# Kernel optimization log

Measured on AMD Instinct MI355X. Metric: run time of the kernel, lower is better.

## Reference

```python
import jax, jax.numpy as jnp
import numpy as np

B, C, N, K = 2, 128, 4096, 16
DIM, PH, AH = 256, 64, 1024  # dim, pos_hidden_dim, dim*attn_hidden_multiplier
EPS = 1e-5

def _p(k, shape, scale=0.02):
    return jax.random.normal(k, shape, dtype=jnp.float32) * scale

def setup_inputs() -> dict:
    key0 = jax.random.key(0)
    ks = jax.random.split(key0, 32)
    d = {
        'pos': jax.random.normal(ks[0], (B, 3, N), dtype=jnp.float32),
        'key': jax.random.normal(ks[1], (B, C, N), dtype=jnp.float32),
        'query': jax.random.normal(ks[2], (B, C, N), dtype=jnp.float32),
        # MLP_Res on concat(key,query): in=2C, hidden=C, out=C
        'mlpv_w1': _p(ks[3], (C, 2 * C)), 'mlpv_b1': jnp.zeros((C,)),
        'mlpv_w2': _p(ks[4], (C, C)),     'mlpv_b2': jnp.zeros((C,)),
        'mlpv_ws': _p(ks[5], (C, 2 * C)), 'mlpv_bs': jnp.zeros((C,)),
        'wk': _p(ks[6], (DIM, C)), 'bk': jnp.zeros((DIM,)),
        'wq': _p(ks[7], (DIM, C)), 'bq': jnp.zeros((DIM,)),
        'wv': _p(ks[8], (DIM, C)), 'bv': jnp.zeros((DIM,)),
        # pos_mlp: Conv2d(3,PH,1) -> BN -> ReLU -> Conv2d(PH,DIM,1)
        'pos_w1': _p(ks[9], (PH, 3)),   'pos_b1': jnp.zeros((PH,)),
        'pos_g1': jnp.ones((PH,)),      'pos_be1': jnp.zeros((PH,)),
        'pos_w2': _p(ks[10], (DIM, PH)),'pos_b2': jnp.zeros((DIM,)),
        # attn_mlp: Conv2d(DIM,AH,1) -> BN -> ReLU -> Conv2d(AH,DIM,1)
        'att_w1': _p(ks[11], (AH, DIM)), 'att_b1': jnp.zeros((AH,)),
        'att_g1': jnp.ones((AH,)),       'att_be1': jnp.zeros((AH,)),
        'att_w2': _p(ks[12], (DIM, AH)), 'att_b2': jnp.zeros((DIM,)),
        'we': _p(ks[13], (C, DIM)), 'be': jnp.zeros((C,)),
    }
    return d

def conv1d(w, b, x):  # 1x1 conv: (o,i),(B,i,N)->(B,o,N)
    return jnp.einsum('oi,bin->bon', w, x) + b[None, :, None]

def conv2d(w, b, x):  # 1x1 conv: (o,i),(B,i,N,K)->(B,o,N,K)
    return jnp.einsum('oi,bink->bonk', w, x) + b[None, :, None, None]

def bn2d(g, be, x):  # training-mode batchnorm over (B,N,K) per channel
    m = x.mean(axis=(0, 2, 3), keepdims=True)
    v = x.var(axis=(0, 2, 3), keepdims=True)
    return g[None, :, None, None] * (x - m) * jax.lax.rsqrt(v + EPS) + be[None, :, None, None]

def knn_idx(pos, k):  # pos: (B,3,N) -> idx (B,N,k) of k nearest (incl. self)
    sq = jnp.sum(pos * pos, axis=1)                      # (B,N)
    d2 = sq[:, :, None] + sq[:, None, :] - 2.0 * jnp.einsum('bdn,bdm->bnm', pos, pos)
    _, idx = jax.lax.top_k(-d2, k)                       # smallest distances
    return idx

def group(x, idx):  # x:(B,C,N), idx:(B,N,K) -> (B,C,N,K)
    return jax.vmap(lambda xb, ib: xb[:, ib])(x, idx)

def reference(pos, key, query,
              mlpv_w1, mlpv_b1, mlpv_w2, mlpv_b2, mlpv_ws, mlpv_bs,
              wk, bk, wq, bq, wv, bv,
              pos_w1, pos_b1, pos_g1, pos_be1, pos_w2, pos_b2,
              att_w1, att_b1, att_g1, att_be1, att_w2, att_b2,
              we, be):
    x = jnp.concatenate([key, query], axis=1)            # (B,2C,N)
    value = conv1d(mlpv_w2, mlpv_b2, jax.nn.relu(conv1d(mlpv_w1, mlpv_b1, x))) \
            + conv1d(mlpv_ws, mlpv_bs, x)                # MLP_Res -> (B,C,N)
    identity = value
    k_f = conv1d(wk, bk, key)                            # (B,DIM,N)
    q_f = conv1d(wq, bq, query)
    v_f = conv1d(wv, bv, value)
    idx = knn_idx(pos, K)                                # (B,N,K)
    key_g = group(k_f, idx)                              # (B,DIM,N,K)
    qk_rel = q_f[:, :, :, None] - key_g
    pos_rel = pos[:, :, :, None] - group(pos, idx)       # (B,3,N,K)
    pos_emb = conv2d(pos_w2, pos_b2,
                     jax.nn.relu(bn2d(pos_g1, pos_be1, conv2d(pos_w1, pos_b1, pos_rel))))
    attn = conv2d(att_w2, att_b2,
                  jax.nn.relu(bn2d(att_g1, att_be1, conv2d(att_w1, att_b1, qk_rel + pos_emb))))
    attn = jax.nn.softmax(attn, axis=-1)                 # softmax over K neighbors
    v = v_f[:, :, :, None] + pos_emb                     # (B,DIM,N,K)
    agg = jnp.einsum('bcik,bcik->bci', attn, v)          # (B,DIM,N)
    y = conv1d(we, be, agg)
    return y + identity
```

## Files before the change

kernel.cpp:

```cpp
#include <hip/hip_runtime.h>
#include <math.h>

#define BB 2
#define CC 128
#define NN 4096
#define KK 16
#define DIMD 256
#define PHH 64
#define AHH 1024
#define EPSF 1e-5f
#define RSPLIT 256
#define RKCH ((BB * NN * KK) / RSPLIT)
#define LSTR 258
#define KNN_CAP 512
#define FPT 8

typedef unsigned short ushort_t;
typedef unsigned char uchar_t;
typedef unsigned long long u64;
typedef long long i64;
typedef __attribute__((ext_vector_type(8))) short short8;
typedef __attribute__((ext_vector_type(8))) unsigned short u16x8;
typedef __attribute__((ext_vector_type(4))) unsigned short u16x4;
typedef __attribute__((ext_vector_type(2))) unsigned short u16x2;
typedef __attribute__((ext_vector_type(4))) float f32x4;

__device__ __forceinline__ ushort_t f2b(float x) {
    union { float f; unsigned u; } v; v.f = x;
    unsigned r = v.u + 0x7fff + ((v.u >> 16) & 1);
    return (ushort_t)(r >> 16);
}
__device__ __forceinline__ float b2f(ushort_t x) {
    union { unsigned u; float f; } v; v.u = ((unsigned)x) << 16;
    return v.f;
}
__device__ __forceinline__ unsigned fsort(float x) {
    union { float f; unsigned u; } v; v.f = x;
    return v.u ^ ((v.u >> 31) ? 0xFFFFFFFFu : 0x80000000u);
}
__device__ __forceinline__ uchar_t f2f8(float x) {
    int p = __builtin_amdgcn_cvt_pk_fp8_f32(x, x, 0, false);
    return (uchar_t)(p & 0xFF);
}

#define GLDS16(gp, lp) __builtin_amdgcn_global_load_lds( \
    (const __attribute__((address_space(1))) void*)(gp), \
    (__attribute__((address_space(3))) void*)(lp), 16, 0, 0)

__global__ void zero_kernel(float* p, int n) {
    int i = blockIdx.x * blockDim.x + threadIdx.x;
    if (i < n) p[i] = 0.f;
}

__global__ __launch_bounds__(256) void knn_kernel(const float* __restrict__ pos,
                                                  int* __restrict__ idx) {
    int bid = blockIdx.x;
    int b = bid / NN, n = bid % NN;
    int t = threadIdx.x;
    int lane = t & 63, w = t >> 6;
    const float* px = pos + (size_t)b * 3 * NN;
    const float* py = px + NN;
    const float* pz = px + 2 * NN;
    float qx = px[n], qy = py[n], qz = pz[n];
    float qs = qx * qx + qy * qy + qz * qz;

    u64 keys[KK];
    u64 lmin = ~0ull;
#pragma unroll
    for (int j = 0; j < KK; ++j) {
        int m = t + 256 * j;
        float mx = px[m], my = py[m], mz = pz[m];
        float ms = mx * mx + my * my + mz * mz;
        float dt = qx * mx + qy * my + qz * mz;
        float d = qs + ms - 2.f * dt;
        u64 k = ((u64)fsort(d) << 32) | (unsigned)m;
        keys[j] = k;
        lmin = k < lmin ? k : lmin;
    }

    __shared__ u64 T0s[4];
    __shared__ u64 pool[KNN_CAP];
    __shared__ int cnt;

    u64 k = lmin, m4 = 0;
#pragma unroll
    for (int r = 0; r < 4; ++r) {
        u64 mv = k;
#pragma unroll
        for (int off = 32; off >= 1; off >>= 1) {
            u64 o = __shfl_xor(mv, off);
            mv = o < mv ? o : mv;
        }
        if (r == 3) m4 = mv;
        if (k == mv) k = ~0ull;
    }
    if (lane == 0) T0s[w] = m4;
    if (t == 0) cnt = 0;
    __syncthreads();
    u64 T0 = T0s[0];
    T0 = T0s[1] > T0 ? T0s[1] : T0;
    T0 = T0s[2] > T0 ? T0s[2] : T0;
    T0 = T0s[3] > T0 ? T0s[3] : T0;

#pragma unroll
    for (int j = 0; j < KK; ++j) {
        if (keys[j] <= T0) {
            int p = atomicAdd(&cnt, 1);
            if (p < KNN_CAP) pool[p] = keys[j];
        }
    }
    __syncthreads();
    int C = cnt < KNN_CAP ? cnt : KNN_CAP;
    if (t < C) {
        u64 me = pool[t];
        int r = 0;
        for (int i = 0; i < C; ++i) r += (pool[i] < me);
        if (r < KK) idx[(size_t)bid * KK + r] = (int)(me & 0xFFFFFFFFu);
    }
}

__global__ __launch_bounds__(256) void cvtx_kernel(const float* __restrict__ key,
                                                   const float* __restrict__ query,
                                                   ushort_t* __restrict__ kqT) {
    __shared__ float xs[128][65];
    int b = blockIdx.y, n0 = blockIdx.x * 64, t = threadIdx.x;
    for (int h = 0; h < 2; ++h) {
        const float* src = (h ? query : key) + (size_t)b * CC * NN;
        if (h) __syncthreads();
#pragma unroll
        for (int it = 0; it < 32; ++it) {
            int l = it * 256 + t;
            xs[l >> 6][l & 63] = src[(size_t)(l >> 6) * NN + n0 + (l & 63)];
        }
        __syncthreads();
#pragma unroll
        for (int it = 0; it < 8; ++it) {
            int l = it * 256 + t;
            int row = l >> 5, c0 = (l & 31) * 4;
            u16x4 pk;
            pk[0] = f2b(xs[c0][row]);
            pk[1] = f2b(xs[c0 + 1][row]);
            pk[2] = f2b(xs[c0 + 2][row]);
            pk[3] = f2b(xs[c0 + 3][row]);
            *(u16x4*)(kqT + ((size_t)b * NN + n0 + row) * 256 + h * 128 + c0) = pk;
        }
    }
}

template <int KLOOP, int ASTR, int EPI, int OSTR>
__global__ __launch_bounds__(256) void gemmT_kernel(const ushort_t* __restrict__ A,
                                                    const ushort_t* __restrict__ Bm,
                                                    const float* __restrict__ bias,
                                                    float* __restrict__ outF,
                                                    ushort_t* __restrict__ outB) {
    __shared__ ushort_t lA[128 * 32];
    __shared__ ushort_t lB[128 * 32];
    int t = threadIdx.x, lane = t & 63, w = t >> 6;
    int wr = w >> 1, wc = w & 1;
    size_t row0 = (size_t)blockIdx.x * 128;
    int col0 = blockIdx.y * 128;
    int m16 = lane & 15, kg = lane >> 4;
    f32x4 acc[4][4];
#pragma unroll
    for (int i = 0; i < 4; ++i)
#pragma unroll
        for (int j = 0; j < 4; ++j) acc[i][j] = (f32x4){0.f, 0.f, 0.f, 0.f};

    const ushort_t* gA = A + (row0 + (size_t)w * 16 + m16) * ASTR + kg * 8;
    const ushort_t* gB = Bm + ((size_t)(col0 + w * 16 + m16)) * KLOOP + kg * 8;
    ushort_t* lA0 = lA + w * 512;
    ushort_t* lB0 = lB + w * 512;
    for (int kt = 0; kt < KLOOP / 32; ++kt) {
        int ko = kt * 32;
        GLDS16(gA + ko, lA0);
        GLDS16(gA + (size_t)64 * ASTR + ko, lA0 + 2048);
        GLDS16(gB + ko, lB0);
        GLDS16(gB + (size_t)64 * KLOOP + ko, lB0 + 2048);
        __syncthreads();
        short8 af[4], bf[4];
#pragma unroll
        for (int i = 0; i < 4; ++i) {
            af[i] = *(const short8*)(lA + ((wr * 4 + i) * 512 + kg * 128 + m16 * 8));
            bf[i] = *(const short8*)(lB + ((wc * 4 + i) * 512 + kg * 128 + m16 * 8));
        }
#pragma unroll
        for (int i = 0; i < 4; ++i)
#pragma unroll
            for (int j = 0; j < 4; ++j)
                acc[i][j] = __builtin_amdgcn_mfma_f32_16x16x32_bf16(af[i], bf[j], acc[i][j], 0, 0, 0);
        __syncthreads();
    }
#pragma unroll
    for (int j = 0; j < 4; ++j) {
        int n = col0 + wc * 64 + j * 16 + m16;
        float bi = bias[n];
#pragma unroll
        for (int i = 0; i < 4; ++i) {
            size_t r = row0 + wr * 64 + i * 16 + kg * 4;
#pragma unroll
            for (int rg = 0; rg < 4; ++rg) {
                float v = acc[i][j][rg] + bi;
                if (EPI == 0) outB[(r + rg) * (size_t)OSTR + n] = f2b(fmaxf(v, 0.f));
                else          outF[(r + rg) * (size_t)OSTR + n] = v;
            }
        }
    }
}

__global__ __launch_bounds__(256) void gemmval_kernel(const ushort_t* __restrict__ kqT,
                                                      const ushort_t* __restrict__ h1T,
                                                      const ushort_t* __restrict__ wsb,
                                                      const ushort_t* __restrict__ w2vb,
                                                      const float* __restrict__ b2,
                                                      const float* __restrict__ bs,
                                                      float* __restrict__ valueTf,
                                                      ushort_t* __restrict__ valueTb) {
    __shared__ ushort_t lA[128 * 32];
    __shared__ ushort_t lB[128 * 32];
    int t = threadIdx.x, lane = t & 63, w = t >> 6;
    int wr = w >> 1, wc = w & 1;
    size_t row0 = (size_t)blockIdx.x * 128;
    int m16 = lane & 15, kg = lane >> 4;
    f32x4 acc[4][4];
#pragma unroll
    for (int i = 0; i < 4; ++i)
#pragma unroll
        for (int j = 0; j < 4; ++j) acc[i][j] = (f32x4){0.f, 0.f, 0.f, 0.f};
    ushort_t* lA0 = lA + w * 512;
    ushort_t* lB0 = lB + w * 512;

    {
        const ushort_t* gA = kqT + (row0 + (size_t)w * 16 + m16) * 256 + kg * 8;
        const ushort_t* gB = wsb + ((size_t)(w * 16 + m16)) * 256 + kg * 8;
        for (int kt = 0; kt < 8; ++kt) {
            int ko = kt * 32;
            GLDS16(gA + ko, lA0);
            GLDS16(gA + (size_t)64 * 256 + ko, lA0 + 2048);
            GLDS16(gB + ko, lB0);
            GLDS16(gB + (size_t)64 * 256 + ko, lB0 + 2048);
            __syncthreads();
            short8 af[4], bf[4];
#pragma unroll
            for (int i = 0; i < 4; ++i) {
                af[i] = *(const short8*)(lA + ((wr * 4 + i) * 512 + kg * 128 + m16 * 8));
                bf[i] = *(const short8*)(lB + ((wc * 4 + i) * 512 + kg * 128 + m16 * 8));
            }
#pragma unroll
            for (int i = 0; i < 4; ++i)
#pragma unroll
                for (int j = 0; j < 4; ++j)
                    acc[i][j] = __builtin_amdgcn_mfma_f32_16x16x32_bf16(af[i], bf[j], acc[i][j], 0, 0, 0);
            __syncthreads();
        }
    }
    {
        const ushort_t* gA = h1T + (row0 + (size_t)w * 16 + m16) * 128 + kg * 8;
        const ushort_t* gB = w2vb + ((size_t)(w * 16 + m16)) * 128 + kg * 8;
        for (int kt = 0; kt < 4; ++kt) {
            int ko = kt * 32;
            GLDS16(gA + ko, lA0);
            GLDS16(gA + (size_t)64 * 128 + ko, lA0 + 2048);
            GLDS16(gB + ko, lB0);
            GLDS16(gB + (size_t)64 * 128 + ko, lB0 + 2048);
            __syncthreads();
            short8 af[4], bf[4];
#pragma unroll
            for (int i = 0; i < 4; ++i) {
                af[i] = *(const short8*)(lA + ((wr * 4 + i) * 512 + kg * 128 + m16 * 8));
                bf[i] = *(const short8*)(lB + ((wc * 4 + i) * 512 + kg * 128 + m16 * 8));
            }
#pragma unroll
            for (int i = 0; i < 4; ++i)
#pragma unroll
                for (int j = 0; j < 4; ++j)
                    acc[i][j] = __builtin_amdgcn_mfma_f32_16x16x32_bf16(af[i], bf[j], acc[i][j], 0, 0, 0);
            __syncthreads();
        }
    }
#pragma unroll
    for (int j = 0; j < 4; ++j) {
        int n = wc * 64 + j * 16 + m16;
        float bi = b2[n] + bs[n];
#pragma unroll
        for (int i = 0; i < 4; ++i) {
            size_t r = row0 + wr * 64 + i * 16 + kg * 4;
#pragma unroll
            for (int rg = 0; rg < 4; ++rg) {
                float v = acc[i][j][rg] + bi;
                valueTf[(r + rg) * (size_t)CC + n] = v;
                valueTb[(r + rg) * (size_t)CC + n] = f2b(v);
            }
        }
    }
}

__global__ __launch_bounds__(256) void gemmkq_kernel(const ushort_t* __restrict__ kqT,
                                                     const ushort_t* __restrict__ wkb,
                                                     const ushort_t* __restrict__ wqb,
                                                     const float* __restrict__ bk,
                                                     const float* __restrict__ bq,
                                                     float* __restrict__ kT,
                                                     float* __restrict__ qT) {
    __shared__ ushort_t lA[128 * 32];
    __shared__ ushort_t lB[128 * 32];
    int half = blockIdx.y >> 1;
    int col0 = (blockIdx.y & 1) * 128;
    const ushort_t* A = kqT + half * 128;
    const ushort_t* Bm = half ? wqb : wkb;
    const float* bias = half ? bq : bk;
    float* outF = half ? qT : kT;

    int t = threadIdx.x, lane = t & 63, w = t >> 6;
    int wr = w >> 1, wc = w & 1;
    size_t row0 = (size_t)blockIdx.x * 128;
    int m16 = lane & 15, kg = lane >> 4;
    f32x4 acc[4][4];
#pragma unroll
    for (int i = 0; i < 4; ++i)
#pragma unroll
        for (int j = 0; j < 4; ++j) acc[i][j] = (f32x4){0.f, 0.f, 0.f, 0.f};
    const ushort_t* gA = A + (row0 + (size_t)w * 16 + m16) * 256 + kg * 8;
    const ushort_t* gB = Bm + ((size_t)(col0 + w * 16 + m16)) * 128 + kg * 8;
    ushort_t* lA0 = lA + w * 512;
    ushort_t* lB0 = lB + w * 512;
    for (int kt = 0; kt < 4; ++kt) {
        int ko = kt * 32;
        GLDS16(gA + ko, lA0);
        GLDS16(gA + (size_t)64 * 256 + ko, lA0 + 2048);
        GLDS16(gB + ko, lB0);
        GLDS16(gB + (size_t)64 * 128 + ko, lB0 + 2048);
        __syncthreads();
        short8 af[4], bf[4];
#pragma unroll
        for (int i = 0; i < 4; ++i) {
            af[i] = *(const short8*)(lA + ((wr * 4 + i) * 512 + kg * 128 + m16 * 8));
            bf[i] = *(const short8*)(lB + ((wc * 4 + i) * 512 + kg * 128 + m16 * 8));
        }
#pragma unroll
        for (int i = 0; i < 4; ++i)
#pragma unroll
            for (int j = 0; j < 4; ++j)
                acc[i][j] = __builtin_amdgcn_mfma_f32_16x16x32_bf16(af[i], bf[j], acc[i][j], 0, 0, 0);
        __syncthreads();
    }
#pragma unroll
    for (int j = 0; j < 4; ++j) {
        int n = col0 + wc * 64 + j * 16 + m16;
        float bi = bias[n];
#pragma unroll
        for (int i = 0; i < 4; ++i) {
            size_t r = row0 + wr * 64 + i * 16 + kg * 4;
#pragma unroll
            for (int rg = 0; rg < 4; ++rg)
                outF[(r + rg) * (size_t)DIMD + n] = acc[i][j][rg] + bi;
        }
    }
}

__global__ __launch_bounds__(256) void pos_stats_kernel(const float* __restrict__ pos,
                                                        const int* __restrict__ idx,
                                                        float* __restrict__ stats) {
    int sid = blockIdx.x * 256 + threadIdx.x;
    int b = sid / (NN * KK);
    int r = sid % (NN * KK);
    int n = r / KK;
    int m = idx[sid];
    const float* px = pos + (size_t)b * 3 * NN;
    float dx = px[n] - px[m];
    float dy = px[NN + n] - px[NN + m];
    float dz = px[2 * NN + n] - px[2 * NN + m];
    float v[9] = {dx, dy, dz, dx * dx, dy * dy, dz * dz, dx * dy, dx * dz, dy * dz};
    __shared__ float red[256];
    for (int j = 0; j < 9; ++j) {
        red[threadIdx.x] = v[j];
        __syncthreads();
        for (int off = 128; off >= 1; off >>= 1) {
            if (threadIdx.x < off) red[threadIdx.x] += red[threadIdx.x + off];
            __syncthreads();
        }
        if (threadIdx.x == 0) atomicAdd(&stats[j], red[0]);
        __syncthreads();
    }
}

__global__ void pos_bn_kernel(const float* __restrict__ stats, const float* __restrict__ pw1,
                              const float* __restrict__ pb1, const float* __restrict__ pg1,
                              const float* __restrict__ pbe1, float* __restrict__ posA) {
    int c = threadIdx.x;
    if (c >= PHH) return;
    float M = (float)(BB * NN * KK);
    float mu0 = stats[0] / M, mu1 = stats[1] / M, mu2 = stats[2] / M;
    float E00 = stats[3] / M, E11 = stats[4] / M, E22 = stats[5] / M;
    float E01 = stats[6] / M, E02 = stats[7] / M, E12 = stats[8] / M;
    float w0 = pw1[c * 3], w1 = pw1[c * 3 + 1], w2 = pw1[c * 3 + 2];
    float wmu = w0 * mu0 + w1 * mu1 + w2 * mu2;
    float mean_h = wmu + pb1[c];
    float Eh2 = w0 * w0 * E00 + w1 * w1 * E11 + w2 * w2 * E22
              + 2.f * (w0 * w1 * E01 + w0 * w2 * E02 + w1 * w2 * E12)
              + 2.f * pb1[c] * wmu + pb1[c] * pb1[c];
    float var = Eh2 - mean_h * mean_h;
    float a1 = pg1[c] * rsqrtf(var + EPSF);
    posA[c] = a1;
    posA[PHH + c] = pbe1[c] - mean_h * a1;
}

__global__ __launch_bounds__(256) void p1_kernel(const float* __restrict__ pos,
                                                 const int* __restrict__ idx,
                                                 const float* __restrict__ pw1,
                                                 const float* __restrict__ pb1,
                                                 const float* __restrict__ posA,
                                                 ushort_t* __restrict__ p1) {
    int gid = blockIdx.x * 256 + threadIdx.x;
    int samp = gid >> 6, c = gid & 63;
    int p = samp >> 4;
    int b = p >> 12, n = p & (NN - 1);
    int m = idx[samp];
    const float* px = pos + (size_t)b * 3 * NN;
    float dx = px[n] - px[m];
    float dy = px[NN + n] - px[NN + m];
    float dz = px[2 * NN + n] - px[2 * NN + m];
    float h = pw1[c * 3] * dx + pw1[c * 3 + 1] * dy + pw1[c * 3 + 2] * dz + pb1[c];
    p1[gid] = f2b(fmaxf(h * posA[c] + posA[PHH + c], 0.f));
}

__global__ __launch_bounds__(1024) void rg_kernel(const ushort_t* __restrict__ S,
                                                  float* __restrict__ Rpart,
                                                  float* __restrict__ mu) {
    __shared__ ushort_t ls[32 * LSTR];
    __shared__ float fmu[DIMD];
    int t = threadIdx.x;
    int lane = t & 63, w = t >> 6;
    int ti = w >> 3, tj = (w >> 2) & 1;
    int wr = (w >> 1) & 1, wc = w & 1;
    int m16 = lane & 15, kg = lane >> 4;
    size_t kbase = (size_t)blockIdx.x * RKCH;

    if (t < DIMD) fmu[t] = 0.f;

    f32x4 acc[4][4];
#pragma unroll
    for (int i = 0; i < 4; ++i)
#pragma unroll
        for (int j = 0; j < 4; ++j) acc[i][j] = (f32x4){0.f, 0.f, 0.f, 0.f};

    int lm = t >> 5;
    int lc = (t & 31) * 8;
    const ushort_t* gS = S + (kbase + lm) * DIMD + lc;
    ushort_t* lp = ls + lm * LSTR + lc;
    float csum[8];
#pragma unroll
    for (int c = 0; c < 8; ++c) csum[c] = 0.f;

    for (int kt = 0; kt < RKCH / 32; ++kt) {
        u16x8 v = *(const u16x8*)(gS + (size_t)kt * 32 * DIMD);
        __syncthreads();
#pragma unroll
        for (int q = 0; q < 4; ++q)
            *(u16x2*)(lp + 2 * q) = (u16x2){v[2 * q], v[2 * q + 1]};
#pragma unroll
        for (int c = 0; c < 8; ++c) csum[c] += b2f(v[c]);
        __syncthreads();
        short8 af[4], bf[4];
#pragma unroll
        for (int i = 0; i < 4; ++i) {
            int chA = ti * 128 + wr * 64 + i * 16 + m16;
            int chB = tj * 128 + wc * 64 + i * 16 + m16;
#pragma unroll
            for (int j = 0; j < 8; ++j) {
                int k = kg * 8 + j;
                af[i][j] = (short)ls[k * LSTR + chA];
                bf[i][j] = (short)ls[k * LSTR + chB];
            }
        }
#pragma unroll
        for (int i = 0; i < 4; ++i)
#pragma unroll
            for (int j = 0; j < 4; ++j)
                acc[i][j] = __builtin_amdgcn_mfma_f32_16x16x32_bf16(af[i], bf[j], acc[i][j], 0, 0, 0);
    }

    float* rp = Rpart + (size_t)blockIdx.x * (DIMD * DIMD);
#pragma unroll
    for (int i = 0; i < 4; ++i) {
        int r0 = ti * 128 + wr * 64 + i * 16 + kg * 4;
#pragma unroll
        for (int j = 0; j < 4; ++j) {
            int cn = tj * 128 + wc * 64 + j * 16 + m16;
#pragma unroll
            for (int rg = 0; rg < 4; ++rg)
                rp[(size_t)(r0 + rg) * DIMD + cn] = acc[i][j][rg];
        }
    }

    __syncthreads();
#pragma unroll
    for (int c = 0; c < 8; ++c) atomicAdd(&fmu[lc + c], csum[c]);
    __syncthreads();
    if (t < DIMD) atomicAdd(&mu[t], fmu[t]);
}

__global__ __launch_bounds__(256) void r_reduce_kernel(const float* __restrict__ Rpart,
                                                       float* __restrict__ R) {
    int e = blockIdx.x * 256 + threadIdx.x;
    float s = 0.f;
    for (int p = 0; p < RSPLIT; ++p) s += Rpart[(size_t)p * (DIMD * DIMD) + e];
    R[e] = s;
}

__global__ __launch_bounds__(256) void attn_bn_kernel(const float* __restrict__ R,
                                                      const float* __restrict__ mu,
                                                      const float* __restrict__ aw1,
                                                      const float* __restrict__ ab1,
                                                      const float* __restrict__ ag1,
                                                      const float* __restrict__ abe1,
                                                      float* __restrict__ attA) {
    int c = blockIdx.x;
    int t = threadIdx.x;
    __shared__ float wsh[DIMD];
    __shared__ float red[DIMD];
    wsh[t] = aw1[(size_t)c * DIMD + t];
    __syncthreads();
    const float* Rr = R + (size_t)t * DIMD;
    float q = 0.f;
#pragma unroll 4
    for (int j = 0; j < DIMD; ++j) q += Rr[j] * wsh[j];
    red[t] = q * wsh[t];
    __syncthreads();
    for (int off = 128; off >= 1; off >>= 1) {
        if (t < off) red[t] += red[t + off];
        __syncthreads();
    }
    float wRw = red[0];
    __syncthreads();
    red[t] = wsh[t] * mu[t];
    __syncthreads();
    for (int off = 128; off >= 1; off >>= 1) {
        if (t < off) red[t] += red[t + off];
        __syncthreads();
    }
    if (t == 0) {
        float M = (float)(BB * NN * KK);
        float wmu = red[0] / M;
        float b1c = ab1[c];
        float Eh = wmu + b1c;
        float Eh2 = wRw / M + 2.f * b1c * wmu + b1c * b1c;
        float var = Eh2 - Eh * Eh;
        float a1 = ag1[c] * rsqrtf(var + EPSF);
        attA[c] = a1;
        attA[AHH + c] = a1 * b1c + abe1[c] - Eh * a1;
    }
}

__global__ void cvt_w_kernel(const float* __restrict__ aw1, const float* __restrict__ aw2,
                             const float* __restrict__ pw2,
                             const float* __restrict__ mw1, const float* __restrict__ mws,
                             const float* __restrict__ mw2,
                             const float* __restrict__ wk, const float* __restrict__ wq,
                             const float* __restrict__ wv,
                             ushort_t* __restrict__ w1b, ushort_t* __restrict__ w2b,
                             ushort_t* __restrict__ pw2b,
                             ushort_t* __restrict__ w1vb, ushort_t* __restrict__ wsvb,
                             ushort_t* __restrict__ w2vb,
                             ushort_t* __restrict__ wkb, ushort_t* __restrict__ wqb,
                             ushort_t* __restrict__ wvb,
                             uchar_t* __restrict__ w2f8) {
    int i = blockIdx.x * 256 + threadIdx.x;
    int o = i;
    if (o < 262144) { w1b[o] = f2b(aw1[o]); return; }   o -= 262144;
    if (o < 262144) { w2b[o] = f2b(aw2[o]); w2f8[o] = f2f8(aw2[o] * 64.f); return; } o -= 262144;
    if (o < 16384)  { pw2b[o] = f2b(pw2[o]); return; }  o -= 16384;
    if (o < 32768)  { w1vb[o] = f2b(mw1[o]); return; }  o -= 32768;
    if (o < 32768)  { wsvb[o] = f2b(mws[o]); return; }  o -= 32768;
    if (o < 16384)  { w2vb[o] = f2b(mw2[o]); return; }  o -= 16384;
    if (o < 32768)  { wkb[o] = f2b(wk[o]); return; }    o -= 32768;
    if (o < 32768)  { wqb[o] = f2b(wq[o]); return; }    o -= 32768;
    if (o < 32768)  { wvb[o] = f2b(wv[o]); }
}

template <int KDIM>
__global__ __launch_bounds__(256) void gemmS_kernel(const ushort_t* __restrict__ A,
                                                    const ushort_t* __restrict__ Bm,
                                                    const float* __restrict__ p0,
                                                    ushort_t* __restrict__ Sb,
                                                    const float* __restrict__ qT,
                                                    const float* __restrict__ kT,
                                                    const int* __restrict__ gidx) {
    __shared__ ushort_t lA[128 * 32];
    __shared__ ushort_t lB[128 * 32];
    int t = threadIdx.x;
    int lane = t & 63, w = t >> 6;
    int wr = w >> 1, wc = w & 1;
    size_t row0 = (size_t)blockIdx.x * 128;
    int col0 = blockIdx.y * 128;
    int m16 = lane & 15, kg = lane >> 4;

    f32x4 acc[4][4];
#pragma unroll
    for (int i = 0; i < 4; ++i)
#pragma unroll
        for (int j = 0; j < 4; ++j) acc[i][j] = (f32x4){0.f, 0.f, 0.f, 0.f};

    const ushort_t* gA = A + (row0 + (size_t)w * 16 + m16) * KDIM + kg * 8;
    const ushort_t* gB = Bm + ((size_t)(col0 + w * 16 + m16)) * KDIM + kg * 8;
    ushort_t* lA0 = lA + w * 512;
    ushort_t* lB0 = lB + w * 512;

    for (int kt = 0; kt < KDIM / 32; ++kt) {
        int ko = kt * 32;
        GLDS16(gA + ko, lA0);
        GLDS16(gA + (size_t)64 * KDIM + ko, lA0 + 2048);
        GLDS16(gB + ko, lB0);
        GLDS16(gB + (size_t)64 * KDIM + ko, lB0 + 2048);
        __syncthreads();
        short8 af[4], bf[4];
#pragma unroll
        for (int i = 0; i < 4; ++i) {
            af[i] = *(const short8*)(lA + ((wr * 4 + i) * 512 + kg * 128 + m16 * 8));
            bf[i] = *(const short8*)(lB + ((wc * 4 + i) * 512 + kg * 128 + m16 * 8));
        }
#pragma unroll
        for (int i = 0; i < 4; ++i)
#pragma unroll
            for (int j = 0; j < 4; ++j)
                acc[i][j] = __builtin_amdgcn_mfma_f32_16x16x32_bf16(af[i], bf[j], acc[i][j], 0, 0, 0);
        __syncthreads();
    }

    int nn[4]; float bi[4];
#pragma unroll
    for (int j = 0; j < 4; ++j) { nn[j] = col0 + wc * 64 + j * 16 + m16; bi[j] = p0[nn[j]]; }
#pragma unroll
    for (int i = 0; i < 4; ++i) {
        size_t r = row0 + wr * 64 + i * 16 + kg * 4;
#pragma unroll
        for (int rg = 0; rg < 4; ++rg) {
            size_t rr = r + rg;
            int p = (int)(rr >> 4);
            int krow = (p & ~(NN - 1)) + gidx[rr];
            const float* qrow = qT + (size_t)p * DIMD;
            const float* kro = kT + (size_t)krow * DIMD;
#pragma unroll
            for (int j = 0; j < 4; ++j) {
                float sv = qrow[nn[j]] - kro[nn[j]] + acc[i][j][rg] + bi[j];
                Sb[rr * (size_t)DIMD + nn[j]] = f2b(sv);
            }
        }
    }
}

__global__ __launch_bounds__(256, 3) void fused_mlp_kernel(const ushort_t* __restrict__ S,
                                                        const ushort_t* __restrict__ w1b,
                                                        const uchar_t* __restrict__ w2f8,
                                                        const float* __restrict__ attA,
                                                        const float* __restrict__ ab2,
                                                        const int* __restrict__ idx,
                                                        const float* __restrict__ qT,
                                                        const float* __restrict__ kT,
                                                        const float* __restrict__ vT,
                                                        float* __restrict__ aggT) {
    __shared__ char smem[49152];
    ushort_t* lS  = (ushort_t*)smem;
    uchar_t*  lHt = (uchar_t*)(smem + 32768);
    ushort_t* lgB = (ushort_t*)smem;

    int t = threadIdx.x;
    int lane = t & 63, w = t >> 6;
    int m16 = lane & 15, kg = lane >> 4;
    size_t row0 = (size_t)blockIdx.x * 64;

#pragma unroll
    for (int i = 0; i < 8; ++i) {
        int lb = w * 8 + i;
        int kt = lb >> 2, st = lb & 3;
        const ushort_t* gp = S + (row0 + st * 16 + m16) * DIMD + kt * 32 + kg * 8;
        GLDS16(gp, lS + lb * 512);
    }

    f32x4 acc2[4][4];
#pragma unroll
    for (int i = 0; i < 4; ++i)
#pragma unroll
        for (int j = 0; j < 4; ++j) acc2[i][j] = (f32x4){0.f, 0.f, 0.f, 0.f};

    __syncthreads();

    for (int jc = 0; jc < 8; ++jc) {
        uchar_t* lHb = lHt + (jc & 1) * 8192;
        f32x4 acc1[2][4];
#pragma unroll
        for (int hi = 0; hi < 2; ++hi)
#pragma unroll
            for (int sj = 0; sj < 4; ++sj) acc1[hi][sj] = (f32x4){0.f, 0.f, 0.f, 0.f};
        const ushort_t* wrow = w1b + ((size_t)(jc * 128 + w * 32 + m16)) * DIMD + kg * 8;
#pragma unroll
        for (int kt = 0; kt < 8; ++kt) {
            short8 af[2], bf[4];
            af[0] = *(const short8*)(wrow + kt * 32);
            af[1] = *(const short8*)(wrow + (size_t)16 * DIMD + kt * 32);
#pragma unroll
            for (int sj = 0; sj < 4; ++sj)
                bf[sj] = *(const short8*)(lS + (kt * 4 + sj) * 512 + kg * 128 + m16 * 8);
            __builtin_amdgcn_s_setprio(1);
#pragma unroll
            for (int hi = 0; hi < 2; ++hi)
#pragma unroll
                for (int sj = 0; sj < 4; ++sj)
                    acc1[hi][sj] = __builtin_amdgcn_mfma_f32_16x16x32_bf16(af[hi], bf[sj], acc1[hi][sj], 0, 0, 0);
            __builtin_amdgcn_s_setprio(0);
        }
#pragma unroll
        for (int hi = 0; hi < 2; ++hi) {
            float4 sc4 = *(const float4*)(attA + jc * 128 + w * 32 + hi * 16 + kg * 4);
            float4 of4 = *(const float4*)(attA + AHH + jc * 128 + w * 32 + hi * 16 + kg * 4);
#pragma unroll
            for (int sj = 0; sj < 4; ++sj) {
                float h0 = fmaxf(sc4.x * acc1[hi][sj][0] + of4.x, 0.f);
                float h1 = fmaxf(sc4.y * acc1[hi][sj][1] + of4.y, 0.f);
                float h2 = fmaxf(sc4.z * acc1[hi][sj][2] + of4.z, 0.f);
                float h3 = fmaxf(sc4.w * acc1[hi][sj][3] + of4.w, 0.f);
                int p01 = __builtin_amdgcn_cvt_pk_fp8_f32(h0, h1, 0, false);
                int pk = __builtin_amdgcn_cvt_pk_fp8_f32(h2, h3, p01, true);
                int ah = (w * 4 + sj) * 512 + (hi * 2 + (kg >> 1)) * 128 + m16 * 8 + (kg & 1) * 4;
                *(int*)(lHb + ah) = pk;
            }
        }
        __syncthreads();
#pragma unroll
        for (int gh = 0; gh < 2; ++gh) {
            i64 af2[8];
#pragma unroll
            for (int gq = 0; gq < 2; ++gq)
#pragma unroll
                for (int oi = 0; oi < 4; ++oi)
                    af2[gq * 4 + oi] = *(const i64*)(w2f8 + ((size_t)(w * 64 + oi * 16 + m16)) * AHH + jc * 128 + (gh * 2 + gq) * 32 + kg * 8);
#pragma unroll
            for (int gq = 0; gq < 2; ++gq) {
                i64 bf2[4];
#pragma unroll
                for (int sj = 0; sj < 4; ++sj)
                    bf2[sj] = *(const i64*)(lHb + ((gh * 2 + gq) * 4 + sj) * 512 + kg * 128 + m16 * 8);
                __builtin_amdgcn_s_setprio(1);
#pragma unroll
                for (int oi = 0; oi < 4; ++oi)
#pragma unroll
                    for (int sj = 0; sj < 4; ++sj)
                        acc2[oi][sj] = __builtin_amdgcn_mfma_f32_16x16x32_fp8_fp8(af2[gq * 4 + oi], bf2[sj], acc2[oi][sj], 0, 0, 0);
                __builtin_amdgcn_s_setprio(0);
            }
        }
    }
    __syncthreads();

    const float invsc = 0.015625f;
#pragma unroll
    for (int oi = 0; oi < 4; ++oi) {
        int ob = w * 64 + oi * 16 + kg * 4;
        float4 b2v = *(const float4*)(ab2 + ob);
#pragma unroll
        for (int sj = 0; sj < 4; ++sj) {
            int smp = sj * 16 + m16;
            lgB[(ob + 0) * 72 + smp] = f2b(acc2[oi][sj][0] * invsc + b2v.x);
            lgB[(ob + 1) * 72 + smp] = f2b(acc2[oi][sj][1] * invsc + b2v.y);
            lgB[(ob + 2) * 72 + smp] = f2b(acc2[oi][sj][2] * invsc + b2v.z);
            lgB[(ob + 3) * 72 + smp] = f2b(acc2[oi][sj][3] * invsc + b2v.w);
        }
    }
    __syncthreads();

    int out = t;
    for (int pt = 0; pt < 4; ++pt) {
        int pid = (int)(row0 >> 4) + pt;
        u16x8 v0 = *(const u16x8*)(lgB + out * 72 + pt * 16);
        u16x8 v1 = *(const u16x8*)(lgB + out * 72 + pt * 16 + 8);
        float lg[KK];
#pragma unroll
        for (int s = 0; s < 8; ++s) { lg[s] = b2f(v0[s]); lg[s + 8] = b2f(v1[s]); }
        float mx = lg[0];
#pragma unroll
        for (int s = 1; s < KK; ++s) mx = fmaxf(mx, lg[s]);
        float se = 0.f;
#pragma unroll
        for (int s = 0; s < KK; ++s) { lg[s] = expf(lg[s] - mx); se += lg[s]; }
        float inv = 1.f / se;
        int base = pid & ~(NN - 1);
        float acc = 0.f;
#pragma unroll
        for (int s = 0; s < KK; ++s) {
            int row = pid * KK + s;
            int krow = base + idx[row];
            float sv = b2f(S[(size_t)row * DIMD + out]);
            float kv = kT[(size_t)krow * DIMD + out];
            acc += lg[s] * (sv + kv);
        }
        float vf = vT[(size_t)pid * DIMD + out];
        float q  = qT[(size_t)pid * DIMD + out];
        aggT[(size_t)pid * DIMD + out] = vf - q + acc * inv;
    }
}

__global__ __launch_bounds__(256) void final_kernel(const float* __restrict__ aggT,
                                                    const float* __restrict__ we,
                                                    const float* __restrict__ be,
                                                    const float* __restrict__ valueTf,
                                                    float* __restrict__ out) {
    __shared__ float xs[2 * FPT][DIMD];
    __shared__ float vs[2 * FPT][CC];
    int b = blockIdx.y;
    int n0 = blockIdx.x * (2 * FPT);
    int t = threadIdx.x;
    const float4* src = (const float4*)(aggT + ((size_t)b * NN + n0) * DIMD);
    float4* dst = (float4*)xs;
#pragma unroll
    for (int l = 0; l < (2 * FPT * DIMD / 4) / 256; ++l) dst[t + 256 * l] = src[t + 256 * l];
    const float4* src2 = (const float4*)(valueTf + ((size_t)b * NN + n0) * CC);
    float4* dst2 = (float4*)vs;
#pragma unroll
    for (int l = 0; l < (2 * FPT * CC / 4) / 256; ++l) dst2[t + 256 * l] = src2[t + 256 * l];
    __syncthreads();
    int o = t & 127, ph = t >> 7;
    float acc[FPT];
#pragma unroll
    for (int p = 0; p < FPT; ++p) acc[p] = 0.f;
    const float4* wr = (const float4*)(we + (size_t)o * DIMD);
#pragma unroll 8
    for (int i4 = 0; i4 < DIMD / 4; ++i4) {
        float4 w4 = wr[i4];
#pragma unroll
        for (int p = 0; p < FPT; ++p) {
            float4 x4 = *(const float4*)&xs[ph * FPT + p][i4 * 4];
            acc[p] += w4.x * x4.x + w4.y * x4.y + w4.z * x4.z + w4.w * x4.w;
        }
    }
    float bo = be[o];
#pragma unroll
    for (int p = 0; p < FPT; ++p) {
        size_t oi = ((size_t)b * CC + o) * NN + n0 + ph * FPT + p;
        out[oi] = acc[p] + bo + vs[ph * FPT + p][o];
    }
}

extern "C" void kernel_launch(void* const* d_in, const int* in_sizes, int n_in,
                              void* d_out, int out_size, void* d_ws, size_t ws_size,
                              hipStream_t stream) {
    (void)in_sizes; (void)n_in; (void)out_size; (void)ws_size;
    const float* pos     = (const float*)d_in[0];
    const float* key     = (const float*)d_in[1];
    const float* query   = (const float*)d_in[2];
    const float* mlpv_w1 = (const float*)d_in[3];
    const float* mlpv_b1 = (const float*)d_in[4];
    const float* mlpv_w2 = (const float*)d_in[5];
    const float* mlpv_b2 = (const float*)d_in[6];
    const float* mlpv_ws = (const float*)d_in[7];
    const float* mlpv_bs = (const float*)d_in[8];
    const float* wk  = (const float*)d_in[9];
    const float* bk  = (const float*)d_in[10];
    const float* wq  = (const float*)d_in[11];
    const float* bq  = (const float*)d_in[12];
    const float* wv  = (const float*)d_in[13];
    const float* bv  = (const float*)d_in[14];
    const float* pw1 = (const float*)d_in[15];
    const float* pb1 = (const float*)d_in[16];
    const float* pg1 = (const float*)d_in[17];
    const float* pbe1= (const float*)d_in[18];
    const float* pw2 = (const float*)d_in[19];
    const float* pb2 = (const float*)d_in[20];
    const float* aw1 = (const float*)d_in[21];
    const float* ab1 = (const float*)d_in[22];
    const float* ag1 = (const float*)d_in[23];
    const float* abe1= (const float*)d_in[24];
    const float* aw2 = (const float*)d_in[25];
    const float* ab2 = (const float*)d_in[26];
    const float* we  = (const float*)d_in[27];
    const float* be  = (const float*)d_in[28];
    float* out = (float*)d_out;

    char* wsb = (char*)d_ws;
    size_t off = 0;
    auto alloc = [&](size_t bytes) {
        void* p = wsb + off;
        off += (bytes + 255) & ~(size_t)255;
        return p;
    };
    const size_t M = (size_t)BB * NN * KK;
    const size_t P = (size_t)BB * NN;
    int*   idx   = (int*)  alloc(M * 4);
    ushort_t* kqT     = (ushort_t*)alloc(P * 256 * 2);
    ushort_t* h1T     = (ushort_t*)alloc(P * CC * 2);
    float*    valueTf = (float*)   alloc(P * CC * 4);
    ushort_t* valueTb = (ushort_t*)alloc(P * CC * 2);
    float* kT    = (float*)alloc(P * DIMD * 4);
    float* qT    = (float*)alloc(P * DIMD * 4);
    float* vT    = (float*)alloc(P * DIMD * 4);
    float* aggT  = (float*)alloc(P * DIMD * 4);
    float* zero0 = (float*)alloc((size_t)(16 + 256 + 65536) * 4);
    float* stats = zero0;
    float* mu    = zero0 + 16;
    float* R     = zero0 + 16 + 256;
    float* posA  = (float*)alloc((size_t)2 * PHH * 4);
    float* attA  = (float*)alloc((size_t)2 * AHH * 4);
    ushort_t* w1b  = (ushort_t*)alloc((size_t)AHH * DIMD * 2);
    ushort_t* w2b  = (ushort_t*)alloc((size_t)DIMD * AHH * 2);
    uchar_t*  w2f8 = (uchar_t*) alloc((size_t)DIMD * AHH);
    ushort_t* pw2b = (ushort_t*)alloc((size_t)DIMD * PHH * 2);
    ushort_t* w1vb = (ushort_t*)alloc((size_t)CC * 256 * 2);
    ushort_t* wsvb = (ushort_t*)alloc((size_t)CC * 256 * 2);
    ushort_t* w2vb = (ushort_t*)alloc((size_t)CC * CC * 2);
    ushort_t* wkb  = (ushort_t*)alloc((size_t)DIMD * CC * 2);
    ushort_t* wqb  = (ushort_t*)alloc((size_t)DIMD * CC * 2);
    ushort_t* wvb  = (ushort_t*)alloc((size_t)DIMD * CC * 2);
    ushort_t* sb16 = (ushort_t*)alloc(M * DIMD * 2);
    char* ovl = (char*)alloc(M * DIMD * 2);
    ushort_t* p1buf = (ushort_t*)ovl;
    float*    Rpart = (float*)ovl;

    int ZN = 16 + 256 + 65536;
    zero_kernel<<<(ZN + 255) / 256, 256, 0, stream>>>(zero0, ZN);
    knn_kernel<<<BB * NN, 256, 0, stream>>>(pos, idx);
    cvt_w_kernel<<<(720896 + 255) / 256, 256, 0, stream>>>(aw1, aw2, pw2, mlpv_w1, mlpv_ws, mlpv_w2,
                                                           wk, wq, wv, w1b, w2b, pw2b,
                                                           w1vb, wsvb, w2vb, wkb, wqb, wvb, w2f8);
    cvtx_kernel<<<dim3(NN / 64, BB), 256, 0, stream>>>(key, query, kqT);
    gemmT_kernel<256, 256, 0, 128><<<dim3(P / 128, 1), 256, 0, stream>>>(kqT, w1vb, mlpv_b1, nullptr, h1T);
    gemmval_kernel<<<dim3(P / 128, 1), 256, 0, stream>>>(kqT, h1T, wsvb, w2vb, mlpv_b2, mlpv_bs, valueTf, valueTb);
    gemmkq_kernel<<<dim3(P / 128, 4), 256, 0, stream>>>(kqT, wkb, wqb, bk, bq, kT, qT);
    gemmT_kernel<128, 128, 1, 256><<<dim3(P / 128, 2), 256, 0, stream>>>(valueTb, wvb, bv, vT, nullptr);
    pos_stats_kernel<<<BB * NN * KK / 256, 256, 0, stream>>>(pos, idx, stats);
    pos_bn_kernel<<<1, 64, 0, stream>>>(stats, pw1, pb1, pg1, pbe1, posA);
    p1_kernel<<<(int)(M * PHH / 256), 256, 0, stream>>>(pos, idx, pw1, pb1, posA, p1buf);
    gemmS_kernel<PHH><<<dim3(M / 128, DIMD / 128), 256, 0, stream>>>(p1buf, pw2b, pb2, sb16, qT, kT, idx);
    rg_kernel<<<RSPLIT, 1024, 0, stream>>>(sb16, Rpart, mu);
    r_reduce_kernel<<<DIMD * DIMD / 256, 256, 0, stream>>>(Rpart, R);
    attn_bn_kernel<<<AHH, DIMD, 0, stream>>>(R, mu, aw1, ab1, ag1, abe1, attA);
    fused_mlp_kernel<<<(int)(M / 64), 256, 0, stream>>>(sb16, w1b, w2f8, attA, ab2, idx, qT, kT, vT, aggT);
    final_kernel<<<dim3(NN / (2 * FPT), BB), 256, 0, stream>>>(aggT, we, be, valueTf, out);
}
```

Measured before the change: 685.8 us.

## Fuse pos-MLP first layer into gemmS and use shuffle reduction for pos stats

Computes the first pos-MLP layer (3->64 conv, BN affine, ReLU) directly inside the gemmS kernel's A-tile load instead of materialising it in a separate buffer. This removes the p1 kernel and its large bf16 intermediate write and reread. The pos_stats reduction switches from nine shared-memory tree reductions to wave shuffles, and the zeroing kernel no longer clears the R buffer. The cost is recomputing the small layer per column block in gemmS.

```diff
diff --git a/kernel.cpp b/kernel.cpp
--- a/kernel.cpp
+++ b/kernel.cpp
@@ -370,16 +370,20 @@
     float dy = px[NN + n] - px[NN + m];
     float dz = px[2 * NN + n] - px[2 * NN + m];
     float v[9] = {dx, dy, dz, dx * dx, dy * dy, dz * dz, dx * dy, dx * dz, dy * dz};
-    __shared__ float red[256];
+    __shared__ float lsum[4][9];
+    int lane = threadIdx.x & 63, w = threadIdx.x >> 6;
+#pragma unroll
     for (int j = 0; j < 9; ++j) {
-        red[threadIdx.x] = v[j];
-        __syncthreads();
-        for (int off = 128; off >= 1; off >>= 1) {
-            if (threadIdx.x < off) red[threadIdx.x] += red[threadIdx.x + off];
-            __syncthreads();
-        }
-        if (threadIdx.x == 0) atomicAdd(&stats[j], red[0]);
-        __syncthreads();
+        float x = v[j];
+#pragma unroll
+        for (int off = 32; off >= 1; off >>= 1) x += __shfl_xor(x, off);
+        if (lane == 0) lsum[w][j] = x;
+    }
+    __syncthreads();
+    if (threadIdx.x < 9) {
+        float s = lsum[0][threadIdx.x] + lsum[1][threadIdx.x]
+                + lsum[2][threadIdx.x] + lsum[3][threadIdx.x];
+        atomicAdd(&stats[threadIdx.x], s);
     }
 }
 
@@ -402,25 +406,6 @@
     float a1 = pg1[c] * rsqrtf(var + EPSF);
     posA[c] = a1;
     posA[PHH + c] = pbe1[c] - mean_h * a1;
-}
-
-__global__ __launch_bounds__(256) void p1_kernel(const float* __restrict__ pos,
-                                                 const int* __restrict__ idx,
-                                                 const float* __restrict__ pw1,
-                                                 const float* __restrict__ pb1,
-                                                 const float* __restrict__ posA,
-                                                 ushort_t* __restrict__ p1) {
-    int gid = blockIdx.x * 256 + threadIdx.x;
-    int samp = gid >> 6, c = gid & 63;
-    int p = samp >> 4;
-    int b = p >> 12, n = p & (NN - 1);
-    int m = idx[samp];
-    const float* px = pos + (size_t)b * 3 * NN;
-    float dx = px[n] - px[m];
-    float dy = px[NN + n] - px[NN + m];
-    float dz = px[2 * NN + n] - px[2 * NN + m];
-    float h = pw1[c * 3] * dx + pw1[c * 3 + 1] * dy + pw1[c * 3 + 2] * dz + pb1[c];
-    p1[gid] = f2b(fmaxf(h * posA[c] + posA[PHH + c], 0.f));
 }
 
 __global__ __launch_bounds__(1024) void rg_kernel(const ushort_t* __restrict__ S,
@@ -577,16 +562,20 @@
     if (o < 32768)  { wvb[o] = f2b(wv[o]); }
 }
 
-template <int KDIM>
-__global__ __launch_bounds__(256) void gemmS_kernel(const ushort_t* __restrict__ A,
+__global__ __launch_bounds__(256) void gemmS_kernel(const float* __restrict__ pos,
+                                                    const int* __restrict__ gidx,
+                                                    const float* __restrict__ pw1,
+                                                    const float* __restrict__ pb1,
+                                                    const float* __restrict__ posA,
                                                     const ushort_t* __restrict__ Bm,
                                                     const float* __restrict__ p0,
                                                     ushort_t* __restrict__ Sb,
                                                     const float* __restrict__ qT,
-                                                    const float* __restrict__ kT,
-                                                    const int* __restrict__ gidx) {
+                                                    const float* __restrict__ kT) {
     __shared__ ushort_t lA[128 * 32];
     __shared__ ushort_t lB[128 * 32];
+    __shared__ float ld3[128][4];
+    __shared__ float pc[64][6];
     int t = threadIdx.x;
     int lane = t & 63, w = t >> 6;
     int wr = w >> 1, wc = w & 1;
@@ -594,23 +583,48 @@
     int col0 = blockIdx.y * 128;
     int m16 = lane & 15, kg = lane >> 4;
 
+    if (t < 64) {
+        pc[t][0] = pw1[t * 3]; pc[t][1] = pw1[t * 3 + 1]; pc[t][2] = pw1[t * 3 + 2];
+        pc[t][3] = pb1[t];     pc[t][4] = posA[t];        pc[t][5] = posA[PHH + t];
+    }
+    if (t < 128) {
+        int row = (int)row0 + t;
+        int m = gidx[row];
+        int p = row >> 4;
+        int b = p >> 12, n = p & (NN - 1);
+        const float* px = pos + (size_t)b * 3 * NN;
+        ld3[t][0] = px[n] - px[m];
+        ld3[t][1] = px[NN + n] - px[NN + m];
+        ld3[t][2] = px[2 * NN + n] - px[2 * NN + m];
+    }
+
     f32x4 acc[4][4];
 #pragma unroll
     for (int i = 0; i < 4; ++i)
 #pragma unroll
         for (int j = 0; j < 4; ++j) acc[i][j] = (f32x4){0.f, 0.f, 0.f, 0.f};
 
-    const ushort_t* gA = A + (row0 + (size_t)w * 16 + m16) * KDIM + kg * 8;
-    const ushort_t* gB = Bm + ((size_t)(col0 + w * 16 + m16)) * KDIM + kg * 8;
-    ushort_t* lA0 = lA + w * 512;
+    const ushort_t* gB = Bm + ((size_t)(col0 + w * 16 + m16)) * PHH + kg * 8;
     ushort_t* lB0 = lB + w * 512;
-
-    for (int kt = 0; kt < KDIM / 32; ++kt) {
+    __syncthreads();
+
+    for (int kt = 0; kt < 2; ++kt) {
         int ko = kt * 32;
-        GLDS16(gA + ko, lA0);
-        GLDS16(gA + (size_t)64 * KDIM + ko, lA0 + 2048);
         GLDS16(gB + ko, lB0);
-        GLDS16(gB + (size_t)64 * KDIM + ko, lB0 + 2048);
+        GLDS16(gB + (size_t)64 * PHH + ko, lB0 + 2048);
+#pragma unroll
+        for (int half = 0; half < 2; ++half) {
+            int rl = half * 64 + w * 16 + m16;
+            float dx = ld3[rl][0], dy = ld3[rl][1], dz = ld3[rl][2];
+            u16x8 pk;
+#pragma unroll
+            for (int j = 0; j < 8; ++j) {
+                int c = ko + kg * 8 + j;
+                float h = pc[c][0] * dx + pc[c][1] * dy + pc[c][2] * dz + pc[c][3];
+                pk[j] = f2b(fmaxf(h * pc[c][4] + pc[c][5], 0.f));
+            }
+            *(u16x8*)(lA + w * 512 + half * 2048 + lane * 8) = pk;
+        }
         __syncthreads();
         short8 af[4], bf[4];
 #pragma unroll
@@ -910,11 +924,10 @@
     ushort_t* wvb  = (ushort_t*)alloc((size_t)DIMD * CC * 2);
     ushort_t* sb16 = (ushort_t*)alloc(M * DIMD * 2);
     char* ovl = (char*)alloc(M * DIMD * 2);
-    ushort_t* p1buf = (ushort_t*)ovl;
-    float*    Rpart = (float*)ovl;
-
-    int ZN = 16 + 256 + 65536;
-    zero_kernel<<<(ZN + 255) / 256, 256, 0, stream>>>(zero0, ZN);
+    float* Rpart = (float*)ovl;
+
+    int ZN = 16 + 256;
+    zero_kernel<<<2, 256, 0, stream>>>(zero0, ZN);
     knn_kernel<<<BB * NN, 256, 0, stream>>>(pos, idx);
     cvt_w_kernel<<<(720896 + 255) / 256, 256, 0, stream>>>(aw1, aw2, pw2, mlpv_w1, mlpv_ws, mlpv_w2,
                                                            wk, wq, wv, w1b, w2b, pw2b,
@@ -926,8 +939,8 @@
     gemmT_kernel<128, 128, 1, 256><<<dim3(P / 128, 2), 256, 0, stream>>>(valueTb, wvb, bv, vT, nullptr);
     pos_stats_kernel<<<BB * NN * KK / 256, 256, 0, stream>>>(pos, idx, stats);
     pos_bn_kernel<<<1, 64, 0, stream>>>(stats, pw1, pb1, pg1, pbe1, posA);
-    p1_kernel<<<(int)(M * PHH / 256), 256, 0, stream>>>(pos, idx, pw1, pb1, posA, p1buf);
-    gemmS_kernel<PHH><<<dim3(M / 128, DIMD / 128), 256, 0, stream>>>(p1buf, pw2b, pb2, sb16, qT, kT, idx);
+    gemmS_kernel<<<dim3(M / 128, DIMD / 128), 256, 0, stream>>>(pos, idx, pw1, pb1, posA,
+                                                                pw2b, pb2, sb16, qT, kT);
     rg_kernel<<<RSPLIT, 1024, 0, stream>>>(sb16, Rpart, mu);
     r_reduce_kernel<<<DIMD * DIMD / 256, 256, 0, stream>>>(Rpart, R);
     attn_bn_kernel<<<AHH, DIMD, 0, stream>>>(R, mu, aw1, ab1, ag1, abe1, attA);
```

New measurement: 614.0 us. 10.5% less time.
